# Performance work log

Measured on AMD Instinct MI355X. Metric: run time of the kernel, lower is better.

## Reference

```python
import jax, jax.numpy as jnp
import numpy as np

D_MODEL = 1024
NUM_HEADS = 16
MAX_LEN = 512  # chunk_size
BATCH = 2
SEQ_LEN = 2048


def _mha(x, w_in, b_in, w_out, b_out, num_heads):
    """torch.nn.MultiheadAttention (eval mode, self-attn) over the last-but-one axis.
    x: (..., S, d). Packed in-proj weight w_in: (3d, d), out-proj w_out: (d, d)."""
    *batch, S, d = x.shape
    hd = d // num_heads
    qkv = x @ w_in.T + b_in                      # (..., S, 3d)
    q, k, v = jnp.split(qkv, 3, axis=-1)
    def heads(t):
        return t.reshape(*batch, S, num_heads, hd)
    q, k, v = heads(q), heads(k), heads(v)
    scale = 1.0 / np.sqrt(hd).astype(np.float32)
    scores = jnp.einsum('...qhd,...khd->...hqk', q, k) * scale
    attn = jax.nn.softmax(scores, axis=-1)
    o = jnp.einsum('...hqk,...khd->...qhd', attn, v).reshape(*batch, S, d)
    return o @ w_out.T + b_out


def setup_inputs() -> dict:
    key = jax.random.key(0)
    ks = jax.random.split(key, 5)
    d = D_MODEL
    s = 0.02
    return {
        'x': jax.random.normal(ks[0], (BATCH, SEQ_LEN, d), dtype=jnp.float32),
        'w_in_l': jax.random.normal(ks[1], (3 * d, d), dtype=jnp.float32) * s,
        'b_in_l': jnp.zeros((3 * d,), jnp.float32),
        'w_out_l': jax.random.normal(ks[2], (d, d), dtype=jnp.float32) * s,
        'b_out_l': jnp.zeros((d,), jnp.float32),
        'w_in_g': jax.random.normal(ks[3], (3 * d, d), dtype=jnp.float32) * s,
        'b_in_g': jnp.zeros((3 * d,), jnp.float32),
        'w_out_g': jax.random.normal(ks[4], (d, d), dtype=jnp.float32) * s,
        'b_out_g': jnp.zeros((d,), jnp.float32),
    }


def reference(x, w_in_l, b_in_l, w_out_l, b_out_l, w_in_g, b_in_g, w_out_g, b_out_g):
    B, S, d = x.shape
    cs = MAX_LEN
    nc = S // cs
    # (B, nc, cs, d) -> (B, cs, nc, d): for each intra-chunk position, attend across chunks.
    xc = x.reshape(B, nc, cs, d).transpose(0, 2, 1, 3)
    # Vectorized replacement for the python loop over chunk positions:
    # batched MHA with batch (B, cs) and sequence length nc.
    loc = _mha(xc, w_in_l, b_in_l, w_out_l, b_out_l, NUM_HEADS)  # (B, cs, nc, d)
    # Faithful to torch: stack -> (nc, cs, B, d), transpose(1,2) -> (nc, B, cs, d),
    # then raw reshape to (B, S, d) (a layout-reinterpreting view, preserved here).
    loc = loc.transpose(2, 0, 1, 3).reshape(B, S, d)
    # Global full self-attention over the whole sequence.
    return _mha(loc, w_in_g, b_in_g, w_out_g, b_out_g, NUM_HEADS)
```

## Files before the change

### kernel.cpp

```cpp
#include <hip/hip_runtime.h>

#define BB 2
#define SS 2048
#define DD 1024
#define HH 16
#define HD 64
#define CS 512
#define NC 4
#define TD 3072
#define MM 4096

typedef __attribute__((ext_vector_type(8))) short short8;
typedef __attribute__((ext_vector_type(4))) float floatx4;

__device__ __forceinline__ float bf2f(unsigned short h) {
  union { unsigned int u; float f; } v; v.u = ((unsigned int)h) << 16; return v.f;
}
__device__ __forceinline__ unsigned short f2bf(float f) {
  union { float f; unsigned int u; } v; v.f = f;
  unsigned int r = (v.u + 0x7fffu + ((v.u >> 16) & 1u)) >> 16;
  return (unsigned short)r;
}
__device__ __forceinline__ short8 ld8f(const float* p) {
  floatx4 f0 = *(const floatx4*)p;
  floatx4 f1 = *(const floatx4*)(p + 4);
  short8 o;
  o[0] = (short)f2bf(f0[0]); o[1] = (short)f2bf(f0[1]);
  o[2] = (short)f2bf(f0[2]); o[3] = (short)f2bf(f0[3]);
  o[4] = (short)f2bf(f1[0]); o[5] = (short)f2bf(f1[1]);
  o[6] = (short)f2bf(f1[2]); o[7] = (short)f2bf(f1[3]);
  return o;
}
__device__ __forceinline__ short8 scale8_eighth(short8 a) {
  short8 o;
#pragma unroll
  for (int j = 0; j < 8; ++j) o[j] = (short)f2bf(bf2f((unsigned short)a[j]) * 0.125f);
  return o;
}
__device__ __forceinline__ void async16(const void* g, void* l) {
  __builtin_amdgcn_global_load_lds((const __attribute__((address_space(1))) void*)g,
                                   (__attribute__((address_space(3))) void*)l, 16, 0, 0);
}

__global__ __launch_bounds__(256) void cvt_all(
    const float* __restrict__ s0, unsigned short* __restrict__ d0, int n0,
    const float* __restrict__ s1, unsigned short* __restrict__ d1, int n1,
    const float* __restrict__ s2, unsigned short* __restrict__ d2, int n2,
    const float* __restrict__ s3, unsigned short* __restrict__ d3, int n3) {
  int bb = blockIdx.x;
  const float* s; unsigned short* d; int off;
  if (bb < n0) { s = s0; d = d0; off = bb; }
  else if (bb < n0 + n1) { s = s1; d = d1; off = bb - n0; }
  else if (bb < n0 + n1 + n2) { s = s2; d = d2; off = bb - n0 - n1; }
  else { s = s3; d = d3; off = bb - n0 - n1 - n2; }
  int i = (off * 256 + threadIdx.x) * 8;
  *(short8*)(d + i) = ld8f(s + i);
}

__global__ __launch_bounds__(256) void cvt_bf16(const float* __restrict__ in,
                                                unsigned short* __restrict__ out, int n) {
  int i = (blockIdx.x * 256 + threadIdx.x) * 8;
  if (i < n) *(short8*)(out + i) = ld8f(in + i);
}

template <int MT, int C_F32>
__global__ __launch_bounds__(256) void gemm_bt_bias(
    const unsigned short* __restrict__ A, const unsigned short* __restrict__ W,
    const float* __restrict__ bias, void* __restrict__ Cv, int M, int N, int K) {
  constexpr int AI = MT / 32;
  __shared__ unsigned short sA[MT * 64];
  __shared__ unsigned short sB[128 * 64];
  const int tid = threadIdx.x;
  const int wid = tid >> 6, lane = tid & 63;
  const int quad = lane >> 4, l15 = lane & 15;
  const int wm = wid & 1, wn = wid >> 1;
  const int bm = blockIdx.y, bn = blockIdx.x;

  floatx4 acc[AI][4];
#pragma unroll
  for (int i = 0; i < AI; ++i)
#pragma unroll
    for (int j = 0; j < 4; ++j) acc[i][j] = (floatx4){0.f, 0.f, 0.f, 0.f};

  const int rb = tid >> 3;
  const int colsw = ((tid & 7) ^ (rb & 7)) << 3;
  const unsigned short* gA = A + (size_t)(bm * MT + rb) * K + colsw;
  const unsigned short* gW = W + (size_t)(bn * 128 + rb) * K + colsw;
  unsigned short* lA = sA + wid * 512;
  unsigned short* lB = sB + wid * 512;

  for (int k0 = 0; k0 < K; k0 += 64) {
#pragma unroll
    for (int i = 0; i < MT / 32; ++i)
      async16(gA + (size_t)(i * 32) * K + k0, lA + i * 2048);
#pragma unroll
    for (int i = 0; i < 4; ++i)
      async16(gW + (size_t)(i * 32) * K + k0, lB + i * 2048);
    __syncthreads();

#pragma unroll
    for (int kk = 0; kk < 2; ++kk) {
      short8 af[AI], bfr[4];
#pragma unroll
      for (int i = 0; i < AI; ++i) {
        int row = wm * (MT / 2) + i * 16 + l15;
        af[i] = *(const short8*)(sA + row * 64 + ((((kk << 2) | quad) ^ (row & 7)) << 3));
      }
#pragma unroll
      for (int j = 0; j < 4; ++j) {
        int row = wn * 64 + j * 16 + l15;
        bfr[j] = *(const short8*)(sB + row * 64 + ((((kk << 2) | quad) ^ (row & 7)) << 3));
      }
#pragma unroll
      for (int i = 0; i < AI; ++i)
#pragma unroll
        for (int j = 0; j < 4; ++j)
          acc[i][j] = __builtin_amdgcn_mfma_f32_16x16x32_bf16(af[i], bfr[j], acc[i][j], 0, 0, 0);
    }
    __syncthreads();
  }

#pragma unroll
  for (int j = 0; j < 4; ++j) {
    int n = bn * 128 + wn * 64 + j * 16 + l15;
    float bv = bias[n];
#pragma unroll
    for (int i = 0; i < AI; ++i) {
      int mrow = bm * MT + wm * (MT / 2) + i * 16 + quad * 4;
#pragma unroll
      for (int rr = 0; rr < 4; ++rr) {
        float v = acc[i][j][rr] + bv;
        if (C_F32) ((float*)Cv)[(size_t)(mrow + rr) * N + n] = v;
        else ((unsigned short*)Cv)[(size_t)(mrow + rr) * N + n] = f2bf(v);
      }
    }
  }
}

__global__ __launch_bounds__(256) void attn_local(const unsigned short* __restrict__ QKV,
                                                  unsigned short* __restrict__ O) {
  const int tid = threadIdx.x;
  const int wid = tid >> 6, lane = tid & 63;
  const int idx = blockIdx.x * 4 + wid;
  const int h = idx & 15, c = (idx >> 4) & 511, b = idx >> 13;

  float q[NC], k[NC], v[NC];
#pragma unroll
  for (int n = 0; n < NC; ++n) {
    size_t base = (size_t)(b * SS + n * CS + c) * TD + h * HD + lane;
    q[n] = bf2f(QKV[base]);
    k[n] = bf2f(QKV[base + DD]);
    v[n] = bf2f(QKV[base + 2 * DD]);
  }
  float s[NC][NC];
#pragma unroll
  for (int m = 0; m < NC; ++m)
#pragma unroll
    for (int n = 0; n < NC; ++n) {
      float p = q[m] * k[n];
#pragma unroll
      for (int off = 32; off >= 1; off >>= 1) p += __shfl_xor(p, off);
      s[m][n] = p * 0.125f;
    }
#pragma unroll
  for (int m = 0; m < NC; ++m) {
    float mx = fmaxf(fmaxf(s[m][0], s[m][1]), fmaxf(s[m][2], s[m][3]));
    float e[NC], sum = 0.f;
#pragma unroll
    for (int n = 0; n < NC; ++n) { e[n] = __expf(s[m][n] - mx); sum += e[n]; }
    float o = (e[0] * v[0] + e[1] * v[1] + e[2] * v[2] + e[3] * v[3]) / sum;
    O[(size_t)(m * (BB * CS) + b * CS + c) * DD + h * HD + lane] = f2bf(o);
  }
}

__global__ __launch_bounds__(256) void transpose_v(const unsigned short* __restrict__ QKV,
                                                   unsigned short* __restrict__ VT) {
  __shared__ unsigned short sT[64 * 64];
  const int tid = threadIdx.x;
  const int bh = blockIdx.x, b = bh >> 4, h = bh & 15;
  const int s0 = blockIdx.y * 64;
#pragma unroll
  for (int it = 0; it < 2; ++it) {
    int C = it * 256 + tid;
    int t = C >> 3, dc = C & 7;
    short8 v = *(const short8*)(QKV + (size_t)(b * SS + s0 + t) * TD + 2 * DD + h * HD + dc * 8);
    *(short8*)(sT + t * 64 + ((dc ^ (t & 7)) << 3)) = v;
  }
  __syncthreads();
#pragma unroll
  for (int it = 0; it < 2; ++it) {
    int C = it * 256 + tid;
    int d = C >> 3, tc = C & 7;
    short8 o;
#pragma unroll
    for (int j = 0; j < 8; ++j) {
      int t = tc * 8 + j;
      o[j] = (short)sT[t * 64 + (((d >> 3) ^ (t & 7)) << 3) + (d & 7)];
    }
    *(short8*)(VT + ((size_t)(bh * 64 + d)) * SS + s0 + tc * 8) = o;
  }
}

__global__ __launch_bounds__(256) void attn_global(
    const unsigned short* __restrict__ Q, const unsigned short* __restrict__ Kp,
    const unsigned short* __restrict__ VT, unsigned short* __restrict__ O) {
  __shared__ unsigned short sK[2][64 * 64];
  __shared__ unsigned short sVT[2][64 * 64];
  __shared__ unsigned short sP[4][32 * 64];
  __shared__ float lsumBuf[64];
  const int tid = threadIdx.x;
  const int wid = tid >> 6, lane = tid & 63;
  const int quad = lane >> 4, l15 = lane & 15;
  const int qhalf = wid & 1, khalf = wid >> 1;
  const int bh = blockIdx.x;
  const int b = bh >> 4, h = bh & 15;
  const int q0 = blockIdx.y * 64 + qhalf * 32;

  short8 qf[2][2];
#pragma unroll
  for (int g = 0; g < 2; ++g) {
    const unsigned short* qr = Q + (size_t)(b * SS + q0 + g * 16 + l15) * TD + h * HD + quad * 8;
    qf[g][0] = scale8_eighth(*(const short8*)qr);
    qf[g][1] = scale8_eighth(*(const short8*)(qr + 32));
  }

  float lsum[2][4];
  floatx4 oacc[2][4];
#pragma unroll
  for (int g = 0; g < 2; ++g)
#pragma unroll
    for (int s = 0; s < 4; ++s) { lsum[g][s] = 0.f; oacc[g][s] = (floatx4){0.f, 0.f, 0.f, 0.f}; }

  unsigned short* myP = &sP[wid][0];
  const unsigned short* myK = &sK[khalf][0];
  const unsigned short* myV = &sVT[khalf][0];
  const unsigned short* vbase = VT + (size_t)(bh * 64) * SS;

  for (int t = 0; t < 16; ++t) {
#pragma unroll
    for (int kh = 0; kh < 2; ++kh) {
      const int kbase = (kh * 16 + t) * 64;
#pragma unroll
      for (int it = 0; it < 2; ++it) {
        int P = it * 256 + tid;
        int key = P >> 3, dc = P & 7;
        short8 kv = *(const short8*)(Kp + (size_t)(b * SS + kbase + key) * TD + h * HD + dc * 8);
        *(short8*)(&sK[kh][0] + key * 64 + ((dc ^ (key & 7)) << 3)) = kv;
      }
#pragma unroll
      for (int it = 0; it < 2; ++it) {
        int P = it * 256 + tid;
        int dim = P >> 3, kcc = P & 7;
        short8 vv = *(const short8*)(vbase + (size_t)dim * SS + kbase + kcc * 8);
        *(short8*)(&sVT[kh][0] + dim * 64 + ((kcc ^ (dim & 7)) << 3)) = vv;
      }
    }
    __syncthreads();

    floatx4 sacc[2][4];
#pragma unroll
    for (int sub = 0; sub < 4; ++sub) {
      int key = sub * 16 + l15;
      int c0 = (quad ^ (key & 7)) << 3;
      short8 kf0 = *(const short8*)(myK + key * 64 + c0);
      short8 kf1 = *(const short8*)(myK + key * 64 + (c0 ^ 32));
#pragma unroll
      for (int g = 0; g < 2; ++g) {
        floatx4 z = (floatx4){0.f, 0.f, 0.f, 0.f};
        z = __builtin_amdgcn_mfma_f32_16x16x32_bf16(qf[g][0], kf0, z, 0, 0, 0);
        z = __builtin_amdgcn_mfma_f32_16x16x32_bf16(qf[g][1], kf1, z, 0, 0, 0);
        sacc[g][sub] = z;
      }
    }

#pragma unroll
    for (int g = 0; g < 2; ++g)
#pragma unroll
      for (int sub = 0; sub < 4; ++sub) {
        int kc8 = sub * 2 + (l15 >> 3), k7 = l15 & 7;
#pragma unroll
        for (int rr = 0; rr < 4; ++rr) {
          unsigned int u = __float_as_uint(__expf(sacc[g][sub][rr]));
          lsum[g][rr] += __uint_as_float(u & 0xffff0000u);
          int row = g * 16 + quad * 4 + rr;
          myP[row * 64 + ((kc8 ^ (row & 7)) << 3) + k7] = (unsigned short)(u >> 16);
        }
      }
    __asm__ volatile("s_waitcnt lgkmcnt(0)" ::: "memory");

    short8 pf[2][2];
#pragma unroll
    for (int g = 0; g < 2; ++g) {
      int row = g * 16 + l15;
      int sw = row & 7;
#pragma unroll
      for (int c = 0; c < 2; ++c)
        pf[g][c] = *(const short8*)(myP + row * 64 + (((c * 4 + quad) ^ sw) << 3));
    }

#pragma unroll
    for (int sub = 0; sub < 4; ++sub) {
      int n = sub * 16 + l15;
      int v0 = (quad ^ (n & 7)) << 3;
      short8 vt0 = *(const short8*)(myV + n * 64 + v0);
      short8 vt1 = *(const short8*)(myV + n * 64 + (v0 ^ 32));
#pragma unroll
      for (int g = 0; g < 2; ++g) {
        oacc[g][sub] = __builtin_amdgcn_mfma_f32_16x16x32_bf16(pf[g][0], vt0, oacc[g][sub], 0, 0, 0);
        oacc[g][sub] = __builtin_amdgcn_mfma_f32_16x16x32_bf16(pf[g][1], vt1, oacc[g][sub], 0, 0, 0);
      }
    }
    __syncthreads();
  }

  float lred[2][4];
#pragma unroll
  for (int g = 0; g < 2; ++g)
#pragma unroll
    for (int rr = 0; rr < 4; ++rr) {
      float t = lsum[g][rr];
#pragma unroll
      for (int off = 8; off >= 1; off >>= 1) t += __shfl_xor(t, off);
      lred[g][rr] = t;
    }

  float* obuf = (float*)&sP[0][0];
  if (khalf == 1) {
    float* my = obuf + qhalf * 2048;
#pragma unroll
    for (int g = 0; g < 2; ++g)
#pragma unroll
      for (int sub = 0; sub < 4; ++sub)
#pragma unroll
        for (int rr = 0; rr < 4; ++rr)
          my[(g * 16 + quad * 4 + rr) * 64 + sub * 16 + l15] = oacc[g][sub][rr];
    if (l15 == 0)
#pragma unroll
      for (int g = 0; g < 2; ++g)
#pragma unroll
        for (int rr = 0; rr < 4; ++rr)
          lsumBuf[qhalf * 32 + g * 16 + quad * 4 + rr] = lred[g][rr];
  }
  __syncthreads();
  if (khalf == 0) {
    float* my = obuf + qhalf * 2048;
#pragma unroll
    for (int g = 0; g < 2; ++g) {
#pragma unroll
      for (int rr = 0; rr < 4; ++rr)
        lred[g][rr] = 1.f / (lred[g][rr] + lsumBuf[qhalf * 32 + g * 16 + quad * 4 + rr]);
#pragma unroll
      for (int sub = 0; sub < 4; ++sub)
#pragma unroll
        for (int rr = 0; rr < 4; ++rr) {
          float v = oacc[g][sub][rr] + my[(g * 16 + quad * 4 + rr) * 64 + sub * 16 + l15];
          int row = b * SS + q0 + g * 16 + quad * 4 + rr;
          O[(size_t)row * DD + h * HD + sub * 16 + l15] = f2bf(v * lred[g][rr]);
        }
    }
  }
}

extern "C" void kernel_launch(void* const* d_in, const int* in_sizes, int n_in,
                              void* d_out, int out_size, void* d_ws, size_t ws_size,
                              hipStream_t stream) {
  const float* x       = (const float*)d_in[0];
  const float* w_in_l  = (const float*)d_in[1];
  const float* b_in_l  = (const float*)d_in[2];
  const float* w_out_l = (const float*)d_in[3];
  const float* b_out_l = (const float*)d_in[4];
  const float* w_in_g  = (const float*)d_in[5];
  const float* b_in_g  = (const float*)d_in[6];
  const float* w_out_g = (const float*)d_in[7];
  const float* b_out_g = (const float*)d_in[8];

  unsigned short* wsA = (unsigned short*)d_ws;
  unsigned short* wsB = wsA + (size_t)MM * TD;
  unsigned short* dob = (unsigned short*)d_out;
  unsigned short* wbf_out_l = dob;
  unsigned short* wbf_in_g  = dob + (size_t)DD * DD;
  unsigned short* wbf_in_l  = dob + 4 * (size_t)DD * DD;
  unsigned short* o1        = dob + 4 * (size_t)DD * DD;
  unsigned short* vtbuf     = dob;

  dim3 blk(256);
  cvt_all<<<dim3(5632), blk, 0, stream>>>(w_out_l, wbf_out_l, 512,
                                          w_in_g, wbf_in_g, 1536,
                                          w_in_l, wbf_in_l, 1536,
                                          x, wsB, 2048);

  gemm_bt_bias<128, 0><<<dim3(TD / 128, MM / 128), blk, 0, stream>>>(wsB, wbf_in_l, b_in_l, wsA, MM, TD, DD);
  attn_local<<<dim3(BB * CS * HH / 4), blk, 0, stream>>>(wsA, o1);
  gemm_bt_bias<64, 0><<<dim3(DD / 128, MM / 64), blk, 0, stream>>>(o1, wbf_out_l, b_out_l, wsB, MM, DD, DD);
  gemm_bt_bias<128, 0><<<dim3(TD / 128, MM / 128), blk, 0, stream>>>(wsB, wbf_in_g, b_in_g, wsA, MM, TD, DD);
  transpose_v<<<dim3(BB * HH, SS / 64), blk, 0, stream>>>(wsA, vtbuf);
  attn_global<<<dim3(BB * HH, SS / 64), blk, 0, stream>>>(wsA, wsA + DD, vtbuf, wsB);
  cvt_bf16<<<dim3(DD * DD / 2048), blk, 0, stream>>>(w_out_g, wsA, DD * DD);
  gemm_bt_bias<64, 1><<<dim3(DD / 128, MM / 64), blk, 0, stream>>>(wsB, wsA, b_out_g, d_out, MM, DD, DD);
}
```

Measured before the change: 324.3 us.

## Process two query tiles per block in global attention to reuse K/V loads

Each attn_global block now handles 128 queries (two 64-query tiles) instead of 64, reusing every K and V^T tile staged in shared memory for both query tiles. The grid is halved to 32x16 = 512 blocks. This halves global-to-LDS traffic for K/V per query. In exchange it doubles the accumulator registers per thread, which may lower occupancy, and it adds an extra synchronized epilogue pass.

New measurement: 378.1 us. 16.6% more time.

```diff
diff --git a/kernel.cpp b/kernel.cpp
--- a/kernel.cpp
+++ b/kernel.cpp
@@ -214,22 +214,30 @@
   const int qhalf = wid & 1, khalf = wid >> 1;
   const int bh = blockIdx.x;
   const int b = bh >> 4, h = bh & 15;
-  const int q0 = blockIdx.y * 64 + qhalf * 32;
-
-  short8 qf[2][2];
-#pragma unroll
-  for (int g = 0; g < 2; ++g) {
-    const unsigned short* qr = Q + (size_t)(b * SS + q0 + g * 16 + l15) * TD + h * HD + quad * 8;
-    qf[g][0] = scale8_eighth(*(const short8*)qr);
-    qf[g][1] = scale8_eighth(*(const short8*)(qr + 32));
-  }
-
-  float lsum[2][4];
-  floatx4 oacc[2][4];
-#pragma unroll
-  for (int g = 0; g < 2; ++g)
-#pragma unroll
-    for (int s = 0; s < 4; ++s) { lsum[g][s] = 0.f; oacc[g][s] = (floatx4){0.f, 0.f, 0.f, 0.f}; }
+  const int q0 = blockIdx.y * 128 + qhalf * 32;
+
+  short8 qf[2][2][2];
+#pragma unroll
+  for (int qt = 0; qt < 2; ++qt)
+#pragma unroll
+    for (int g = 0; g < 2; ++g) {
+      const unsigned short* qr =
+          Q + (size_t)(b * SS + q0 + qt * 64 + g * 16 + l15) * TD + h * HD + quad * 8;
+      qf[qt][g][0] = scale8_eighth(*(const short8*)qr);
+      qf[qt][g][1] = scale8_eighth(*(const short8*)(qr + 32));
+    }
+
+  float lsum[2][2][4];
+  floatx4 oacc[2][2][4];
+#pragma unroll
+  for (int qt = 0; qt < 2; ++qt)
+#pragma unroll
+    for (int g = 0; g < 2; ++g)
+#pragma unroll
+      for (int s = 0; s < 4; ++s) {
+        lsum[qt][g][s] = 0.f;
+        oacc[qt][g][s] = (floatx4){0.f, 0.f, 0.f, 0.f};
+      }
 
   unsigned short* myP = &sP[wid][0];
   const unsigned short* myK = &sK[khalf][0];
@@ -257,107 +265,117 @@
     }
     __syncthreads();
 
-    floatx4 sacc[2][4];
-#pragma unroll
-    for (int sub = 0; sub < 4; ++sub) {
-      int key = sub * 16 + l15;
-      int c0 = (quad ^ (key & 7)) << 3;
-      short8 kf0 = *(const short8*)(myK + key * 64 + c0);
-      short8 kf1 = *(const short8*)(myK + key * 64 + (c0 ^ 32));
+#pragma unroll
+    for (int qt = 0; qt < 2; ++qt) {
+      floatx4 sacc[2][4];
+#pragma unroll
+      for (int sub = 0; sub < 4; ++sub) {
+        int key = sub * 16 + l15;
+        int c0 = (quad ^ (key & 7)) << 3;
+        short8 kf0 = *(const short8*)(myK + key * 64 + c0);
+        short8 kf1 = *(const short8*)(myK + key * 64 + (c0 ^ 32));
+#pragma unroll
+        for (int g = 0; g < 2; ++g) {
+          floatx4 z = (floatx4){0.f, 0.f, 0.f, 0.f};
+          z = __builtin_amdgcn_mfma_f32_16x16x32_bf16(qf[qt][g][0], kf0, z, 0, 0, 0);
+          z = __builtin_amdgcn_mfma_f32_16x16x32_bf16(qf[qt][g][1], kf1, z, 0, 0, 0);
+          sacc[g][sub] = z;
+        }
+      }
+
+#pragma unroll
+      for (int g = 0; g < 2; ++g)
+#pragma unroll
+        for (int sub = 0; sub < 4; ++sub) {
+          int kc8 = sub * 2 + (l15 >> 3), k7 = l15 & 7;
+#pragma unroll
+          for (int rr = 0; rr < 4; ++rr) {
+            unsigned int u = __float_as_uint(__expf(sacc[g][sub][rr]));
+            lsum[qt][g][rr] += __uint_as_float(u & 0xffff0000u);
+            int row = g * 16 + quad * 4 + rr;
+            myP[row * 64 + ((kc8 ^ (row & 7)) << 3) + k7] = (unsigned short)(u >> 16);
+          }
+        }
+      __asm__ volatile("s_waitcnt lgkmcnt(0)" ::: "memory");
+
+      short8 pf[2][2];
 #pragma unroll
       for (int g = 0; g < 2; ++g) {
-        floatx4 z = (floatx4){0.f, 0.f, 0.f, 0.f};
-        z = __builtin_amdgcn_mfma_f32_16x16x32_bf16(qf[g][0], kf0, z, 0, 0, 0);
-        z = __builtin_amdgcn_mfma_f32_16x16x32_bf16(qf[g][1], kf1, z, 0, 0, 0);
-        sacc[g][sub] = z;
-      }
-    }
-
+        int row = g * 16 + l15;
+        int sw = row & 7;
+#pragma unroll
+        for (int c = 0; c < 2; ++c)
+          pf[g][c] = *(const short8*)(myP + row * 64 + (((c * 4 + quad) ^ sw) << 3));
+      }
+
+#pragma unroll
+      for (int sub = 0; sub < 4; ++sub) {
+        int n = sub * 16 + l15;
+        int v0 = (quad ^ (n & 7)) << 3;
+        short8 vt0 = *(const short8*)(myV + n * 64 + v0);
+        short8 vt1 = *(const short8*)(myV + n * 64 + (v0 ^ 32));
+#pragma unroll
+        for (int g = 0; g < 2; ++g) {
+          oacc[qt][g][sub] =
+              __builtin_amdgcn_mfma_f32_16x16x32_bf16(pf[g][0], vt0, oacc[qt][g][sub], 0, 0, 0);
+          oacc[qt][g][sub] =
+              __builtin_amdgcn_mfma_f32_16x16x32_bf16(pf[g][1], vt1, oacc[qt][g][sub], 0, 0, 0);
+        }
+      }
+    }
+    __syncthreads();
+  }
+
+  float* obuf = (float*)&sP[0][0];
+#pragma unroll
+  for (int qt = 0; qt < 2; ++qt) {
+    float lred[2][4];
 #pragma unroll
     for (int g = 0; g < 2; ++g)
 #pragma unroll
-      for (int sub = 0; sub < 4; ++sub) {
-        int kc8 = sub * 2 + (l15 >> 3), k7 = l15 & 7;
-#pragma unroll
-        for (int rr = 0; rr < 4; ++rr) {
-          unsigned int u = __float_as_uint(__expf(sacc[g][sub][rr]));
-          lsum[g][rr] += __uint_as_float(u & 0xffff0000u);
-          int row = g * 16 + quad * 4 + rr;
-          myP[row * 64 + ((kc8 ^ (row & 7)) << 3) + k7] = (unsigned short)(u >> 16);
-        }
-      }
-    __asm__ volatile("s_waitcnt lgkmcnt(0)" ::: "memory");
-
-    short8 pf[2][2];
-#pragma unroll
-    for (int g = 0; g < 2; ++g) {
-      int row = g * 16 + l15;
-      int sw = row & 7;
-#pragma unroll
-      for (int c = 0; c < 2; ++c)
-        pf[g][c] = *(const short8*)(myP + row * 64 + (((c * 4 + quad) ^ sw) << 3));
-    }
-
-#pragma unroll
-    for (int sub = 0; sub < 4; ++sub) {
-      int n = sub * 16 + l15;
-      int v0 = (quad ^ (n & 7)) << 3;
-      short8 vt0 = *(const short8*)(myV + n * 64 + v0);
-      short8 vt1 = *(const short8*)(myV + n * 64 + (v0 ^ 32));
+      for (int rr = 0; rr < 4; ++rr) {
+        float tr = lsum[qt][g][rr];
+#pragma unroll
+        for (int off = 8; off >= 1; off >>= 1) tr += __shfl_xor(tr, off);
+        lred[g][rr] = tr;
+      }
+
+    if (khalf == 1) {
+      float* my = obuf + qhalf * 2048;
+#pragma unroll
+      for (int g = 0; g < 2; ++g)
+#pragma unroll
+        for (int sub = 0; sub < 4; ++sub)
+#pragma unroll
+          for (int rr = 0; rr < 4; ++rr)
+            my[(g * 16 + quad * 4 + rr) * 64 + sub * 16 + l15] = oacc[qt][g][sub][rr];
+      if (l15 == 0)
+#pragma unroll
+        for (int g = 0; g < 2; ++g)
+#pragma unroll
+          for (int rr = 0; rr < 4; ++rr)
+            lsumBuf[qhalf * 32 + g * 16 + quad * 4 + rr] = lred[g][rr];
+    }
+    __syncthreads();
+    if (khalf == 0) {
+      float* my = obuf + qhalf * 2048;
 #pragma unroll
       for (int g = 0; g < 2; ++g) {
-        oacc[g][sub] = __builtin_amdgcn_mfma_f32_16x16x32_bf16(pf[g][0], vt0, oacc[g][sub], 0, 0, 0);
-        oacc[g][sub] = __builtin_amdgcn_mfma_f32_16x16x32_bf16(pf[g][1], vt1, oacc[g][sub], 0, 0, 0);
-      }
-    }
-    __syncthreads();
-  }
-
-  float lred[2][4];
-#pragma unroll
-  for (int g = 0; g < 2; ++g)
-#pragma unroll
-    for (int rr = 0; rr < 4; ++rr) {
-      float t = lsum[g][rr];
-#pragma unroll
-      for (int off = 8; off >= 1; off >>= 1) t += __shfl_xor(t, off);
-      lred[g][rr] = t;
-    }
-
-  float* obuf = (float*)&sP[0][0];
-  if (khalf == 1) {
-    float* my = obuf + qhalf * 2048;
-#pragma unroll
-    for (int g = 0; g < 2; ++g)
-#pragma unroll
-      for (int sub = 0; sub < 4; ++sub)
+        float inv[4];
 #pragma unroll
         for (int rr = 0; rr < 4; ++rr)
-          my[(g * 16 + quad * 4 + rr) * 64 + sub * 16 + l15] = oacc[g][sub][rr];
-    if (l15 == 0)
-#pragma unroll
-      for (int g = 0; g < 2; ++g)
-#pragma unroll
-        for (int rr = 0; rr < 4; ++rr)
-          lsumBuf[qhalf * 32 + g * 16 + quad * 4 + rr] = lred[g][rr];
-  }
-  __syncthreads();
-  if (khalf == 0) {
-    float* my = obuf + qhalf * 2048;
-#pragma unroll
-    for (int g = 0; g < 2; ++g) {
-#pragma unroll
-      for (int rr = 0; rr < 4; ++rr)
-        lred[g][rr] = 1.f / (lred[g][rr] + lsumBuf[qhalf * 32 + g * 16 + quad * 4 + rr]);
-#pragma unroll
-      for (int sub = 0; sub < 4; ++sub)
-#pragma unroll
-        for (int rr = 0; rr < 4; ++rr) {
-          float v = oacc[g][sub][rr] + my[(g * 16 + quad * 4 + rr) * 64 + sub * 16 + l15];
-          int row = b * SS + q0 + g * 16 + quad * 4 + rr;
-          O[(size_t)row * DD + h * HD + sub * 16 + l15] = f2bf(v * lred[g][rr]);
-        }
-    }
+          inv[rr] = 1.f / (lred[g][rr] + lsumBuf[qhalf * 32 + g * 16 + quad * 4 + rr]);
+#pragma unroll
+        for (int sub = 0; sub < 4; ++sub)
+#pragma unroll
+          for (int rr = 0; rr < 4; ++rr) {
+            float v = oacc[qt][g][sub][rr] + my[(g * 16 + quad * 4 + rr) * 64 + sub * 16 + l15];
+            int row = b * SS + q0 + qt * 64 + g * 16 + quad * 4 + rr;
+            O[(size_t)row * DD + h * HD + sub * 16 + l15] = f2bf(v * inv[rr]);
+          }
+      }
+    }
+    __syncthreads();
   }
 }
 
@@ -394,7 +412,7 @@
   gemm_bt_bias<64, 0><<<dim3(DD / 128, MM / 64), blk, 0, stream>>>(o1, wbf_out_l, b_out_l, wsB, MM, DD, DD);
   gemm_bt_bias<128, 0><<<dim3(TD / 128, MM / 128), blk, 0, stream>>>(wsB, wbf_in_g, b_in_g, wsA, MM, TD, DD);
   transpose_v<<<dim3(BB * HH, SS / 64), blk, 0, stream>>>(wsA, vtbuf);
-  attn_global<<<dim3(BB * HH, SS / 64), blk, 0, stream>>>(wsA, wsA + DD, vtbuf, wsB);
+  attn_global<<<dim3(BB * HH, SS / 128), blk, 0, stream>>>(wsA, wsA + DD, vtbuf, wsB);
   cvt_bf16<<<dim3(DD * DD / 2048), blk, 0, stream>>>(w_out_g, wsA, DD * DD);
   gemm_bt_bias<64, 1><<<dim3(DD / 128, MM / 64), blk, 0, stream>>>(wsB, wsA, b_out_g, d_out, MM, DD, DD);
 }
```

## Keep softmax probabilities in registers and load K/V tiles asynchronously in global attention

Applied to the files above, without the earlier changes.

The QK^T MFMA operands are swapped so the score accumulator layout lines up with the P operand of the PV MFMA. Exponentials are then packed straight into bf16 registers, which removes the per-wave sP shared-memory round trip and its waitcnt. V fragments are gathered with 8-byte LDS reads to match the new key ordering. K/V tile loads now use async16 global-to-LDS copies with precomputed swizzled offsets. The launch bound requests 4 blocks per CU and the output reduction reuses sK as scratch, which lowers LDS use but risks register pressure.

After: 298.7 us. 1.09x faster.

```diff
diff --git a/kernel.cpp b/kernel.cpp
--- a/kernel.cpp
+++ b/kernel.cpp
@@ -12,6 +12,7 @@
 
 typedef __attribute__((ext_vector_type(8))) short short8;
 typedef __attribute__((ext_vector_type(4))) float floatx4;
+typedef __attribute__((ext_vector_type(2))) unsigned int uintx2;
 
 __device__ __forceinline__ float bf2f(unsigned short h) {
   union { unsigned int u; float f; } v; v.u = ((unsigned int)h) << 16; return v.f;
@@ -201,13 +202,12 @@
   }
 }
 
-__global__ __launch_bounds__(256) void attn_global(
+__global__ __launch_bounds__(256, 4) void attn_global(
     const unsigned short* __restrict__ Q, const unsigned short* __restrict__ Kp,
     const unsigned short* __restrict__ VT, unsigned short* __restrict__ O) {
   __shared__ unsigned short sK[2][64 * 64];
   __shared__ unsigned short sVT[2][64 * 64];
-  __shared__ unsigned short sP[4][32 * 64];
-  __shared__ float lsumBuf[64];
+  __shared__ float lsb[2][64];
   const int tid = threadIdx.x;
   const int wid = tid >> 6, lane = tid & 63;
   const int quad = lane >> 4, l15 = lane & 15;
@@ -224,35 +224,34 @@
     qf[g][1] = scale8_eighth(*(const short8*)(qr + 32));
   }
 
-  float lsum[2][4];
+  float lsum[2] = {0.f, 0.f};
   floatx4 oacc[2][4];
 #pragma unroll
   for (int g = 0; g < 2; ++g)
 #pragma unroll
-    for (int s = 0; s < 4; ++s) { lsum[g][s] = 0.f; oacc[g][s] = (floatx4){0.f, 0.f, 0.f, 0.f}; }
-
-  unsigned short* myP = &sP[wid][0];
+    for (int s = 0; s < 4; ++s) oacc[g][s] = (floatx4){0.f, 0.f, 0.f, 0.f};
+
   const unsigned short* myK = &sK[khalf][0];
   const unsigned short* myV = &sVT[khalf][0];
   const unsigned short* vbase = VT + (size_t)(bh * 64) * SS;
 
+  unsigned int koff[2], voff[2];
+#pragma unroll
+  for (int it = 0; it < 2; ++it) {
+    const int P = it * 256 + tid;
+    const int row = P >> 3, s = P & 7;
+    koff[it] = (unsigned int)((b * SS + row) * TD + h * HD + ((s ^ (row & 7)) << 3));
+    voff[it] = (unsigned int)(row * SS + ((s ^ (row & 7)) << 3));
+  }
+
   for (int t = 0; t < 16; ++t) {
 #pragma unroll
     for (int kh = 0; kh < 2; ++kh) {
       const int kbase = (kh * 16 + t) * 64;
 #pragma unroll
       for (int it = 0; it < 2; ++it) {
-        int P = it * 256 + tid;
-        int key = P >> 3, dc = P & 7;
-        short8 kv = *(const short8*)(Kp + (size_t)(b * SS + kbase + key) * TD + h * HD + dc * 8);
-        *(short8*)(&sK[kh][0] + key * 64 + ((dc ^ (key & 7)) << 3)) = kv;
-      }
-#pragma unroll
-      for (int it = 0; it < 2; ++it) {
-        int P = it * 256 + tid;
-        int dim = P >> 3, kcc = P & 7;
-        short8 vv = *(const short8*)(vbase + (size_t)dim * SS + kbase + kcc * 8);
-        *(short8*)(&sVT[kh][0] + dim * 64 + ((kcc ^ (dim & 7)) << 3)) = vv;
+        async16(Kp + (size_t)kbase * TD + koff[it], (unsigned short*)&sK[kh][0] + it * 2048 + wid * 512);
+        async16(vbase + kbase + voff[it], (unsigned short*)&sVT[kh][0] + it * 2048 + wid * 512);
       }
     }
     __syncthreads();
@@ -267,64 +266,76 @@
 #pragma unroll
       for (int g = 0; g < 2; ++g) {
         floatx4 z = (floatx4){0.f, 0.f, 0.f, 0.f};
-        z = __builtin_amdgcn_mfma_f32_16x16x32_bf16(qf[g][0], kf0, z, 0, 0, 0);
-        z = __builtin_amdgcn_mfma_f32_16x16x32_bf16(qf[g][1], kf1, z, 0, 0, 0);
+        z = __builtin_amdgcn_mfma_f32_16x16x32_bf16(kf0, qf[g][0], z, 0, 0, 0);
+        z = __builtin_amdgcn_mfma_f32_16x16x32_bf16(kf1, qf[g][1], z, 0, 0, 0);
         sacc[g][sub] = z;
       }
     }
 
+    short8 pf[2][2];
 #pragma unroll
     for (int g = 0; g < 2; ++g)
 #pragma unroll
-      for (int sub = 0; sub < 4; ++sub) {
-        int kc8 = sub * 2 + (l15 >> 3), k7 = l15 & 7;
-#pragma unroll
-        for (int rr = 0; rr < 4; ++rr) {
-          unsigned int u = __float_as_uint(__expf(sacc[g][sub][rr]));
-          lsum[g][rr] += __uint_as_float(u & 0xffff0000u);
-          int row = g * 16 + quad * 4 + rr;
-          myP[row * 64 + ((kc8 ^ (row & 7)) << 3) + k7] = (unsigned short)(u >> 16);
+      for (int c = 0; c < 2; ++c) {
+        unsigned int w[4];
+#pragma unroll
+        for (int hs = 0; hs < 2; ++hs) {
+          const floatx4 z = sacc[g][2 * c + hs];
+          unsigned int u0 = __float_as_uint(__expf(z[0]));
+          unsigned int u1 = __float_as_uint(__expf(z[1]));
+          unsigned int u2 = __float_as_uint(__expf(z[2]));
+          unsigned int u3 = __float_as_uint(__expf(z[3]));
+          lsum[g] += __uint_as_float(u0 & 0xffff0000u);
+          lsum[g] += __uint_as_float(u1 & 0xffff0000u);
+          lsum[g] += __uint_as_float(u2 & 0xffff0000u);
+          lsum[g] += __uint_as_float(u3 & 0xffff0000u);
+          w[hs * 2 + 0] = (u0 >> 16) | (u1 & 0xffff0000u);
+          w[hs * 2 + 1] = (u2 >> 16) | (u3 & 0xffff0000u);
         }
-      }
-    __asm__ volatile("s_waitcnt lgkmcnt(0)" ::: "memory");
-
-    short8 pf[2][2];
-#pragma unroll
-    for (int g = 0; g < 2; ++g) {
-      int row = g * 16 + l15;
-      int sw = row & 7;
-#pragma unroll
-      for (int c = 0; c < 2; ++c)
-        pf[g][c] = *(const short8*)(myP + row * 64 + (((c * 4 + quad) ^ sw) << 3));
-    }
+        union { unsigned int u[4]; short8 s; } pk;
+        pk.u[0] = w[0]; pk.u[1] = w[1]; pk.u[2] = w[2]; pk.u[3] = w[3];
+        pf[g][c] = pk.s;
+      }
 
 #pragma unroll
     for (int sub = 0; sub < 4; ++sub) {
-      int n = sub * 16 + l15;
-      int v0 = (quad ^ (n & 7)) << 3;
-      short8 vt0 = *(const short8*)(myV + n * 64 + v0);
-      short8 vt1 = *(const short8*)(myV + n * 64 + (v0 ^ 32));
+      const int n = sub * 16 + l15;
+      const int nsw = n & 7;
+      const int inner = (quad & 1) * 4;
+      short8 vb[2];
+#pragma unroll
+      for (int c = 0; c < 2; ++c) {
+        const int c8a = (((c << 2) | (quad >> 1)) ^ nsw);
+        const int c8b = (((c << 2) | 2 | (quad >> 1)) ^ nsw);
+        uintx2 a = *(const uintx2*)(myV + n * 64 + c8a * 8 + inner);
+        uintx2 d = *(const uintx2*)(myV + n * 64 + c8b * 8 + inner);
+        union { unsigned int u[4]; short8 s; } vk;
+        vk.u[0] = a[0]; vk.u[1] = a[1]; vk.u[2] = d[0]; vk.u[3] = d[1];
+        vb[c] = vk.s;
+      }
 #pragma unroll
       for (int g = 0; g < 2; ++g) {
-        oacc[g][sub] = __builtin_amdgcn_mfma_f32_16x16x32_bf16(pf[g][0], vt0, oacc[g][sub], 0, 0, 0);
-        oacc[g][sub] = __builtin_amdgcn_mfma_f32_16x16x32_bf16(pf[g][1], vt1, oacc[g][sub], 0, 0, 0);
+        oacc[g][sub] = __builtin_amdgcn_mfma_f32_16x16x32_bf16(pf[g][0], vb[0], oacc[g][sub], 0, 0, 0);
+        oacc[g][sub] = __builtin_amdgcn_mfma_f32_16x16x32_bf16(pf[g][1], vb[1], oacc[g][sub], 0, 0, 0);
       }
     }
     __syncthreads();
   }
 
-  float lred[2][4];
-#pragma unroll
-  for (int g = 0; g < 2; ++g)
-#pragma unroll
-    for (int rr = 0; rr < 4; ++rr) {
-      float t = lsum[g][rr];
-#pragma unroll
-      for (int off = 8; off >= 1; off >>= 1) t += __shfl_xor(t, off);
-      lred[g][rr] = t;
-    }
-
-  float* obuf = (float*)&sP[0][0];
+  float lh[2];
+#pragma unroll
+  for (int g = 0; g < 2; ++g) {
+    float s = lsum[g];
+    s += __shfl_xor(s, 16);
+    s += __shfl_xor(s, 32);
+    lh[g] = s;
+  }
+  if (lane < 16) {
+#pragma unroll
+    for (int g = 0; g < 2; ++g) lsb[khalf][qhalf * 32 + g * 16 + l15] = lh[g];
+  }
+
+  float* obuf = (float*)&sK[0][0];
   if (khalf == 1) {
     float* my = obuf + qhalf * 2048;
 #pragma unroll
@@ -334,28 +345,25 @@
 #pragma unroll
         for (int rr = 0; rr < 4; ++rr)
           my[(g * 16 + quad * 4 + rr) * 64 + sub * 16 + l15] = oacc[g][sub][rr];
-    if (l15 == 0)
-#pragma unroll
-      for (int g = 0; g < 2; ++g)
-#pragma unroll
-        for (int rr = 0; rr < 4; ++rr)
-          lsumBuf[qhalf * 32 + g * 16 + quad * 4 + rr] = lred[g][rr];
   }
   __syncthreads();
   if (khalf == 0) {
     float* my = obuf + qhalf * 2048;
 #pragma unroll
     for (int g = 0; g < 2; ++g) {
-#pragma unroll
-      for (int rr = 0; rr < 4; ++rr)
-        lred[g][rr] = 1.f / (lred[g][rr] + lsumBuf[qhalf * 32 + g * 16 + quad * 4 + rr]);
+      float inv[4];
+#pragma unroll
+      for (int rr = 0; rr < 4; ++rr) {
+        int idx = qhalf * 32 + g * 16 + quad * 4 + rr;
+        inv[rr] = 1.f / (lsb[0][idx] + lsb[1][idx]);
+      }
 #pragma unroll
       for (int sub = 0; sub < 4; ++sub)
 #pragma unroll
         for (int rr = 0; rr < 4; ++rr) {
           float v = oacc[g][sub][rr] + my[(g * 16 + quad * 4 + rr) * 64 + sub * 16 + l15];
           int row = b * SS + q0 + g * 16 + quad * 4 + rr;
-          O[(size_t)row * DD + h * HD + sub * 16 + l15] = f2bf(v * lred[g][rr]);
+          O[(size_t)row * DD + h * HD + sub * 16 + l15] = f2bf(v * inv[rr]);
         }
     }
   }
```
